# Kernel tuning notes

Measured on AMD Instinct MI355X. Metric: run time of the kernel, lower is better.

The kernel has to match this reference:

```python
import jax, jax.numpy as jnp
import numpy as np

N = 50000      # num vertices
E = 600000     # num incidence pairs
M = 100000     # num hyperedges
IN = 256       # in_channels
H = 8          # heads
C = 32         # out_channels per head


def setup_inputs() -> dict:
    key = jax.random.key(0)
    k = jax.random.split(key, 5)
    X = jax.random.normal(k[0], (N, IN), jnp.float32)
    W = jax.random.normal(k[1], (IN, H * C), jnp.float32) * (1.0 / np.sqrt(IN))
    att_e = jax.random.normal(k[2], (1, H, C), jnp.float32) * 0.1
    vertex = jax.random.randint(k[3], (E,), 0, N)
    edges = jax.random.randint(k[4], (E,), 0, M)
    return {"X": X, "W": W, "att_e": att_e, "vertex": vertex, "edges": edges, "num_edges": M}


def reference(X, W, att_e, vertex, edges, num_edges):
    n, h, c = X.shape[0], att_e.shape[1], att_e.shape[2]
    X0 = X @ W                              # [N, H*C]
    Xh = X0.reshape(n, h, c)                # [N, H, C]
    Xve = Xh[vertex]                        # [E, H, C] gather node feats per incidence
    # mean-aggregate incidences -> hyperedge features
    cnt = jax.ops.segment_sum(jnp.ones((vertex.shape[0],), X.dtype), edges, num_segments=num_edges)
    Xe = jax.ops.segment_sum(Xve, edges, num_segments=num_edges) / jnp.maximum(cnt, 1.0)[:, None, None]  # [M, H, C]
    alpha_e = jnp.sum(Xe * att_e, axis=-1)  # [M, H]
    a_ev = alpha_e[edges]                   # [E, H]
    alpha = jnp.where(a_ev >= 0, a_ev, 0.2 * a_ev)  # leaky_relu(0.2)
    # numerically stable segment softmax over incidences grouped by vertex
    amax = jax.ops.segment_max(alpha, vertex, num_segments=n)[vertex]
    aexp = jnp.exp(alpha - amax)
    asum = jax.ops.segment_sum(aexp, vertex, num_segments=n)[vertex]
    attn = aexp / (asum + 1e-16)            # [E, H]
    Xev = Xe[edges] * attn[:, :, None]      # [E, H, C]
    Xv = jax.ops.segment_sum(Xev, vertex, num_segments=n)  # [N, H, C]
    return jax.nn.gelu(Xv.reshape(n, h * c), approximate=False)
```

## Files before the change

kernel.cpp:

```cpp
#include <hip/hip_runtime.h>
#include <hip/hip_bf16.h>
#include <math.h>

#define NV 50000
#define NE 600000
#define NM 100000
#define KIN 256
#define HCC 256
#define NHH 8

#define NCH 96
#define CHUNK 6250
#define KRANGE 25000
#define NPASS 6
#define HIST_B (NCH * NPASS)
#define CSCAN_B 74

#define SCAN_NB0 25
#define SCAN_NB1 13

#define CNT_B 2344
#define GEMM_RG 784
#define GEMM_B (GEMM_RG * 4)

typedef unsigned int u32;
typedef unsigned short u16;
typedef _Float16 f16;
typedef _Float16 v8h __attribute__((ext_vector_type(8)));
typedef _Float16 v4h __attribute__((ext_vector_type(4)));
typedef float v4f __attribute__((ext_vector_type(4)));
typedef float v8f __attribute__((ext_vector_type(8)));

__global__ __launch_bounds__(256) void k_hist_gemm(const int* __restrict__ vertex,
                                                   const int* __restrict__ edges,
                                                   u16* __restrict__ r_e,
                                                   u16* __restrict__ r_v,
                                                   u16* __restrict__ Ce,
                                                   u16* __restrict__ Cv,
                                                   const float* __restrict__ X,
                                                   const float* __restrict__ W,
                                                   f16* __restrict__ X0) {
    __shared__ __align__(16) u32 smem[KRANGE / 2];
    const int bid = blockIdx.x;
    const int t = threadIdx.x;
    if (bid < HIST_B) {
        u32* hist = smem;
        const int pass = bid / NCH;
        const int chunk = bid % NCH;
        const bool eside = pass < 4;
        const int kbase = (eside ? pass : pass - 4) * KRANGE;
        const int* keys = eside ? edges : vertex;
        u16* rout = eside ? r_e : r_v;
        u16* crow = eside ? (Ce + (size_t)chunk * NM) : (Cv + (size_t)chunk * NV);

        uint4* h4 = (uint4*)hist;
        for (int j = t; j < KRANGE / 8; j += 256) h4[j] = make_uint4(0u, 0u, 0u, 0u);
        __syncthreads();

        const int i0 = chunk * CHUNK;
        for (int i = i0 + t; i < i0 + CHUNK; i += 256) {
            int k = keys[i] - kbase;
            if ((u32)k < (u32)KRANGE) {
                int sh = (k & 1) << 4;
                u32 old = atomicAdd(&hist[k >> 1], 1u << sh);
                rout[i] = (u16)(old >> sh);
            }
        }
        __syncthreads();

        uint4* d4 = (uint4*)(crow + kbase);
        for (int j = t; j < KRANGE / 8; j += 256) d4[j] = h4[j];
        return;
    }
    typedef f16 (*tile_t)[72];
    tile_t sA = (tile_t)smem;
    tile_t sB = (tile_t)((char*)smem + 64 * 72 * 2);
    const int g = bid - HIST_B;
    const int rg = (g >> 5) * 8 + (g & 7);
    const int cg = (g >> 3) & 3;
    if (rg >= (NV + 63) / 64) return;
    const int r0 = rg * 64;
    const int c0 = cg * 64;
    const int wave = t >> 6;
    const int lane = t & 63;
    const int quad = lane >> 4;
    const int l16 = lane & 15;
    const int wr = wave & 1;
    const int wc = wave >> 1;

    v4f acc[2][2] = {{{0.f,0.f,0.f,0.f},{0.f,0.f,0.f,0.f}},
                     {{0.f,0.f,0.f,0.f},{0.f,0.f,0.f,0.f}}};

    for (int kc = 0; kc < KIN; kc += 64) {
        __syncthreads();
        #pragma unroll
        for (int i = 0; i < 4; ++i) {
            int lin = i * 256 + t;
            int row = lin >> 4;
            int k = (lin & 15) * 4;
            int gr = r0 + row;
            float4 x = make_float4(0.f, 0.f, 0.f, 0.f);
            if (gr < NV) x = *(const float4*)(X + (size_t)gr * KIN + kc + k);
            v4h hv = { (f16)x.x, (f16)x.y, (f16)x.z, (f16)x.w };
            *(v4h*)&sA[row][k] = hv;
        }
        #pragma unroll
        for (int i = 0; i < 4; ++i) {
            int lin = i * 256 + t;
            int k = lin >> 4;
            int n = (lin & 15) * 4;
            float4 b = *(const float4*)(W + (size_t)(kc + k) * HCC + c0 + n);
            sB[n + 0][k] = (f16)b.x;
            sB[n + 1][k] = (f16)b.y;
            sB[n + 2][k] = (f16)b.z;
            sB[n + 3][k] = (f16)b.w;
        }
        __syncthreads();
        #pragma unroll
        for (int ks = 0; ks < 2; ++ks) {
            const int kb = ks * 32 + quad * 8;
            v8h a[2], b[2];
            #pragma unroll
            for (int rf = 0; rf < 2; ++rf)
                a[rf] = *(const v8h*)&sA[wr * 32 + rf * 16 + l16][kb];
            #pragma unroll
            for (int cf = 0; cf < 2; ++cf)
                b[cf] = *(const v8h*)&sB[wc * 32 + cf * 16 + l16][kb];
            #pragma unroll
            for (int rf = 0; rf < 2; ++rf)
                #pragma unroll
                for (int cf = 0; cf < 2; ++cf)
                    acc[rf][cf] = __builtin_amdgcn_mfma_f32_16x16x32_f16(a[rf], b[cf], acc[rf][cf], 0, 0, 0);
        }
    }
    #pragma unroll
    for (int rf = 0; rf < 2; ++rf)
        #pragma unroll
        for (int cf = 0; cf < 2; ++cf)
            #pragma unroll
            for (int r = 0; r < 4; ++r) {
                int grow = r0 + wr * 32 + rf * 16 + quad * 4 + r;
                if (grow < NV)
                    X0[(size_t)grow * HCC + c0 + wc * 32 + cf * 16 + l16] = (f16)acc[rf][cf][r];
            }
}

__global__ __launch_bounds__(1024) void k_cscan(u16* __restrict__ Ce,
                                                u16* __restrict__ Cv,
                                                int* __restrict__ e_start,
                                                int* __restrict__ v_start) {
    int tid = blockIdx.x * 1024 + threadIdx.x;
    u32* mat;
    int* outp;
    int col, ncol;
    if (tid < NM / 2)               { mat = (u32*)Ce; outp = e_start; col = tid;          ncol = NM / 2; }
    else if (tid < NM / 2 + NV / 2) { mat = (u32*)Cv; outp = v_start; col = tid - NM / 2; ncol = NV / 2; }
    else return;
    u32 s = 0;
    u32* p = mat + col;
    for (int c = 0; c < NCH; ++c) {
        u32 o = *p;
        *p = s;
        s += o;
        p += ncol;
    }
    outp[2 * col + 1] = (int)(s & 0xffffu);
    outp[2 * col + 2] = (int)(s >> 16);
}

__global__ __launch_bounds__(1024) void k_scan_blk(int* __restrict__ a0,
                                                   int* __restrict__ a1,
                                                   int* __restrict__ bsum) {
    const int b = blockIdx.x;
    int* a;
    int n, base;
    if (b < SCAN_NB0) { a = a0; n = NM + 1; base = b * 4096; }
    else              { a = a1; n = NV + 1; base = (b - SCAN_NB0) * 4096; }
    const int t = threadIdx.x;
    const int lane = t & 63, w = t >> 6;
    const int i = base + t * 4;
    int4 v = make_int4(0, 0, 0, 0);
    if (i + 3 < n) v = *(const int4*)(a + i);
    else if (i < n) {
        v.x = a[i];
        if (i + 1 < n) v.y = a[i + 1];
        if (i + 2 < n) v.z = a[i + 2];
    }
    v.y += v.x; v.z += v.y; v.w += v.z;
    int s = v.w;
    #pragma unroll
    for (int d = 1; d < 64; d <<= 1) {
        int x = __shfl_up(s, d, 64);
        if (lane >= d) s += x;
    }
    __shared__ int partials[16];
    __shared__ int woff[16];
    if (lane == 63) partials[w] = s;
    __syncthreads();
    if (t < 16) {
        int p = partials[t];
        int ps = p;
        #pragma unroll
        for (int d = 1; d < 16; d <<= 1) {
            int x = __shfl_up(ps, d, 64);
            if (t >= d) ps += x;
        }
        woff[t] = ps - p;
        if (t == 15) bsum[b] = ps;
    }
    __syncthreads();
    const int add = (s - v.w) + woff[w];
    v.x += add; v.y += add; v.z += add; v.w += add;
    if (i + 3 < n) *(int4*)(a + i) = v;
    else if (i < n) {
        a[i] = v.x;
        if (i + 1 < n) a[i + 1] = v.y;
        if (i + 2 < n) a[i + 2] = v.z;
    }
}

__global__ __launch_bounds__(1024) void k_scan_add(int* __restrict__ a0,
                                                   int* __restrict__ a1,
                                                   const int* __restrict__ bsum) {
    const int b = blockIdx.x;
    int* a;
    int n, bs0, blocal;
    if (b < SCAN_NB0) { a = a0; n = NM + 1; bs0 = 0;        blocal = b; }
    else              { a = a1; n = NV + 1; bs0 = SCAN_NB0; blocal = b - SCAN_NB0; }
    const int t = threadIdx.x;
    const int lane = t & 63;
    int x = (lane < blocal) ? bsum[bs0 + lane] : 0;
    #pragma unroll
    for (int d = 1; d < 64; d <<= 1) x += __shfl_xor(x, d, 64);
    const int off = x;
    const int i = blocal * 4096 + t * 4;
    if (i + 3 < n) {
        int4 v = *(const int4*)(a + i);
        v.x += off; v.y += off; v.z += off; v.w += off;
        *(int4*)(a + i) = v;
    } else if (i < n) {
        a[i] += off;
        if (i + 1 < n) a[i + 1] += off;
        if (i + 2 < n) a[i + 2] += off;
    }
}

__global__ __launch_bounds__(256) void k_fill2(const int* __restrict__ vertex,
                                               const int* __restrict__ edges,
                                               const u16* __restrict__ r_e,
                                               const u16* __restrict__ r_v,
                                               const int* __restrict__ e_start,
                                               const int* __restrict__ v_start,
                                               const u16* __restrict__ Ce,
                                               const u16* __restrict__ Cv,
                                               int* __restrict__ e_list,
                                               int* __restrict__ v_list) {
    int i = blockIdx.x * 256 + threadIdx.x;
    if (i >= NE) return;
    int v = vertex[i], m = edges[i];
    int chunk = i / CHUNK;
    int pe = e_start[m] + (int)Ce[(size_t)chunk * NM + m] + (int)r_e[i];
    e_list[pe] = v;
    int pv = v_start[v] + (int)Cv[(size_t)chunk * NV + v] + (int)r_v[i];
    v_list[pv] = m;
}

__global__ __launch_bounds__(256) void k_egather(const int* __restrict__ e_start,
                                                 const int* __restrict__ e_list,
                                                 const f16* __restrict__ X0,
                                                 const float* __restrict__ att,
                                                 f16* __restrict__ Xe,
                                                 float* __restrict__ alpha_e) {
    int m = blockIdx.x * 4 + (threadIdx.x >> 6);
    int lane = threadIdx.x & 63;
    int half = lane >> 5;
    int l32 = lane & 31;
    int c8 = l32 * 8;
    int s0 = e_start[m], s1 = e_start[m + 1];
    v8f acc = {0.f,0.f,0.f,0.f,0.f,0.f,0.f,0.f};
    int i = s0 + half;
    for (; i + 2 < s1; i += 4) {
        int v0 = e_list[i], v1 = e_list[i + 2];
        v8h x0 = *(const v8h*)(X0 + (size_t)v0 * HCC + c8);
        v8h x1 = *(const v8h*)(X0 + (size_t)v1 * HCC + c8);
        #pragma unroll
        for (int j = 0; j < 8; ++j) acc[j] += (float)x0[j] + (float)x1[j];
    }
    if (i < s1) {
        int v0 = e_list[i];
        v8h x0 = *(const v8h*)(X0 + (size_t)v0 * HCC + c8);
        #pragma unroll
        for (int j = 0; j < 8; ++j) acc[j] += (float)x0[j];
    }
    #pragma unroll
    for (int j = 0; j < 8; ++j) acc[j] += __shfl_xor(acc[j], 32, 64);
    float inv = 1.0f / fmaxf((float)(s1 - s0), 1.0f);
    #pragma unroll
    for (int j = 0; j < 8; ++j) acc[j] *= inv;
    if (half == 0) {
        v8h xv;
        #pragma unroll
        for (int j = 0; j < 8; ++j) xv[j] = (f16)acc[j];
        *(v8h*)(Xe + (size_t)m * HCC + c8) = xv;
    }
    float4 a0 = *(const float4*)(att + c8);
    float4 a1 = *(const float4*)(att + c8 + 4);
    float p = acc[0]*a0.x + acc[1]*a0.y + acc[2]*a0.z + acc[3]*a0.w
            + acc[4]*a1.x + acc[5]*a1.y + acc[6]*a1.z + acc[7]*a1.w;
    p += __shfl_xor(p, 1, 64);
    p += __shfl_xor(p, 2, 64);
    if (half == 0 && (l32 & 3) == 0) alpha_e[m * NHH + (l32 >> 2)] = p;
}

__global__ __launch_bounds__(256) void k_vgather(const int* __restrict__ v_start,
                                                 const int* __restrict__ v_list,
                                                 const f16* __restrict__ Xe,
                                                 const float* __restrict__ alpha_e,
                                                 float* __restrict__ out) {
    int v = blockIdx.x * 4 + (threadIdx.x >> 6);
    int lane = threadIdx.x & 63;
    int half = lane >> 5;
    int l32 = lane & 31;
    int h = l32 >> 2;
    int c8 = l32 * 8;
    int s0 = v_start[v], s1 = v_start[v + 1];
    v8f acc = {0.f,0.f,0.f,0.f,0.f,0.f,0.f,0.f};
    float se = 0.f;
    int i = s0 + half;
    for (; i + 2 < s1; i += 4) {
        int m0 = v_list[i], m1 = v_list[i + 2];
        float a0 = alpha_e[m0 * NHH + h];
        float a1 = alpha_e[m1 * NHH + h];
        v8h x0 = *(const v8h*)(Xe + (size_t)m0 * HCC + c8);
        v8h x1 = *(const v8h*)(Xe + (size_t)m1 * HCC + c8);
        a0 = (a0 >= 0.f) ? a0 : 0.2f * a0;
        a1 = (a1 >= 0.f) ? a1 : 0.2f * a1;
        float e0 = __expf(a0);
        float e1 = __expf(a1);
        #pragma unroll
        for (int j = 0; j < 8; ++j) acc[j] += e0 * (float)x0[j] + e1 * (float)x1[j];
        se += e0 + e1;
    }
    if (i < s1) {
        int m0 = v_list[i];
        float a0 = alpha_e[m0 * NHH + h];
        v8h x0 = *(const v8h*)(Xe + (size_t)m0 * HCC + c8);
        a0 = (a0 >= 0.f) ? a0 : 0.2f * a0;
        float e0 = __expf(a0);
        #pragma unroll
        for (int j = 0; j < 8; ++j) acc[j] += e0 * (float)x0[j];
        se += e0;
    }
    #pragma unroll
    for (int j = 0; j < 8; ++j) acc[j] += __shfl_xor(acc[j], 32, 64);
    se += __shfl_xor(se, 32, 64);
    if (half) return;
    float inv = 1.0f / (se + 1e-16f);
    float4 o0, o1;
    float xx;
    xx = acc[0] * inv; o0.x = 0.5f * xx * (1.f + erff(xx * 0.70710678118f));
    xx = acc[1] * inv; o0.y = 0.5f * xx * (1.f + erff(xx * 0.70710678118f));
    xx = acc[2] * inv; o0.z = 0.5f * xx * (1.f + erff(xx * 0.70710678118f));
    xx = acc[3] * inv; o0.w = 0.5f * xx * (1.f + erff(xx * 0.70710678118f));
    xx = acc[4] * inv; o1.x = 0.5f * xx * (1.f + erff(xx * 0.70710678118f));
    xx = acc[5] * inv; o1.y = 0.5f * xx * (1.f + erff(xx * 0.70710678118f));
    xx = acc[6] * inv; o1.z = 0.5f * xx * (1.f + erff(xx * 0.70710678118f));
    xx = acc[7] * inv; o1.w = 0.5f * xx * (1.f + erff(xx * 0.70710678118f));
    *(float4*)(out + (size_t)v * HCC + c8) = o0;
    *(float4*)(out + (size_t)v * HCC + c8 + 4) = o1;
}

extern "C" void kernel_launch(void* const* d_in, const int* in_sizes, int n_in,
                              void* d_out, int out_size, void* d_ws, size_t ws_size,
                              hipStream_t stream) {
    const float* X = (const float*)d_in[0];
    const float* W = (const float*)d_in[1];
    const float* att = (const float*)d_in[2];
    const int* vertex = (const int*)d_in[3];
    const int* edges = (const int*)d_in[4];
    float* out = (float*)d_out;

    char* ws = (char*)d_ws;
    size_t off = 0;
    #define WS_TAKE(bytes) (ws + off); off += (((size_t)(bytes)) + 15) & ~(size_t)15
    f16* X0 = (f16*)WS_TAKE((size_t)NV * HCC * 2);
    f16* Xe = (f16*)WS_TAKE((size_t)NM * HCC * 2);
    float* alpha_e = (float*)WS_TAKE((size_t)NM * NHH * 4);
    size_t z0 = off;
    int* e_start = (int*)WS_TAKE((size_t)(NM + 1) * 4);
    int* v_start = (int*)WS_TAKE((size_t)(NV + 1) * 4);
    size_t z1 = off;
    int* e_list = (int*)WS_TAKE((size_t)NE * 4);
    int* v_list = (int*)WS_TAKE((size_t)NE * 4);
    u16* r_e = (u16*)WS_TAKE((size_t)NE * 2);
    u16* r_v = (u16*)WS_TAKE((size_t)NE * 2);
    u16* Ce = (u16*)WS_TAKE((size_t)NCH * NM * 2);
    u16* Cv = (u16*)WS_TAKE((size_t)NCH * NV * 2);
    int* bsum = (int*)WS_TAKE(64 * 4);
    #undef WS_TAKE

    hipMemsetAsync(e_start, 0, z1 - z0, stream);

    k_hist_gemm<<<HIST_B + GEMM_B, 256, 0, stream>>>(vertex, edges, r_e, r_v, Ce, Cv,
                                                     X, W, X0);
    k_cscan<<<CSCAN_B, 1024, 0, stream>>>(Ce, Cv, e_start, v_start);
    k_scan_blk<<<SCAN_NB0 + SCAN_NB1, 1024, 0, stream>>>(e_start, v_start, bsum);
    k_scan_add<<<SCAN_NB0 + SCAN_NB1, 1024, 0, stream>>>(e_start, v_start, bsum);
    k_fill2<<<CNT_B, 256, 0, stream>>>(vertex, edges, r_e, r_v, e_start, v_start,
                                       Ce, Cv, e_list, v_list);
    k_egather<<<NM / 4, 256, 0, stream>>>(e_start, e_list, X0, att, Xe, alpha_e);
    k_vgather<<<NV / 4, 256, 0, stream>>>(v_start, v_list, Xe, alpha_e, out);
}
```

Before: 329.5 us.

## Move GEMM into fill kernel, shrink histogram chunk count, trim memset

The X@W GEMM blocks move from the histogram kernel into the fill kernel, so the histogram kernel no longer carries the large shared-memory footprint alongside GEMM tiles and the GEMM overlaps with the scatter fill instead. The chunk count for the per-chunk histograms drops from 96 to 32, which shrinks the Ce/Cv count matrices and the column-scan work but gives fewer, longer histogram blocks. The memset now clears only the first element of each start array, relying on the scan kernels to write the rest.

```diff
diff --git a/kernel.cpp b/kernel.cpp
--- a/kernel.cpp
+++ b/kernel.cpp
@@ -9,8 +9,8 @@
 #define HCC 256
 #define NHH 8
 
-#define NCH 96
-#define CHUNK 6250
+#define NCH 32
+#define CHUNK 18750
 #define KRANGE 25000
 #define NPASS 6
 #define HIST_B (NCH * NPASS)
@@ -31,118 +31,40 @@
 typedef float v4f __attribute__((ext_vector_type(4)));
 typedef float v8f __attribute__((ext_vector_type(8)));
 
-__global__ __launch_bounds__(256) void k_hist_gemm(const int* __restrict__ vertex,
-                                                   const int* __restrict__ edges,
-                                                   u16* __restrict__ r_e,
-                                                   u16* __restrict__ r_v,
-                                                   u16* __restrict__ Ce,
-                                                   u16* __restrict__ Cv,
-                                                   const float* __restrict__ X,
-                                                   const float* __restrict__ W,
-                                                   f16* __restrict__ X0) {
-    __shared__ __align__(16) u32 smem[KRANGE / 2];
+__global__ __launch_bounds__(256) void k_hist(const int* __restrict__ vertex,
+                                              const int* __restrict__ edges,
+                                              u16* __restrict__ r_e,
+                                              u16* __restrict__ r_v,
+                                              u16* __restrict__ Ce,
+                                              u16* __restrict__ Cv) {
+    __shared__ __align__(16) u32 hist[KRANGE / 2];
     const int bid = blockIdx.x;
     const int t = threadIdx.x;
-    if (bid < HIST_B) {
-        u32* hist = smem;
-        const int pass = bid / NCH;
-        const int chunk = bid % NCH;
-        const bool eside = pass < 4;
-        const int kbase = (eside ? pass : pass - 4) * KRANGE;
-        const int* keys = eside ? edges : vertex;
-        u16* rout = eside ? r_e : r_v;
-        u16* crow = eside ? (Ce + (size_t)chunk * NM) : (Cv + (size_t)chunk * NV);
-
-        uint4* h4 = (uint4*)hist;
-        for (int j = t; j < KRANGE / 8; j += 256) h4[j] = make_uint4(0u, 0u, 0u, 0u);
-        __syncthreads();
-
-        const int i0 = chunk * CHUNK;
-        for (int i = i0 + t; i < i0 + CHUNK; i += 256) {
-            int k = keys[i] - kbase;
-            if ((u32)k < (u32)KRANGE) {
-                int sh = (k & 1) << 4;
-                u32 old = atomicAdd(&hist[k >> 1], 1u << sh);
-                rout[i] = (u16)(old >> sh);
-            }
-        }
-        __syncthreads();
-
-        uint4* d4 = (uint4*)(crow + kbase);
-        for (int j = t; j < KRANGE / 8; j += 256) d4[j] = h4[j];
-        return;
-    }
-    typedef f16 (*tile_t)[72];
-    tile_t sA = (tile_t)smem;
-    tile_t sB = (tile_t)((char*)smem + 64 * 72 * 2);
-    const int g = bid - HIST_B;
-    const int rg = (g >> 5) * 8 + (g & 7);
-    const int cg = (g >> 3) & 3;
-    if (rg >= (NV + 63) / 64) return;
-    const int r0 = rg * 64;
-    const int c0 = cg * 64;
-    const int wave = t >> 6;
-    const int lane = t & 63;
-    const int quad = lane >> 4;
-    const int l16 = lane & 15;
-    const int wr = wave & 1;
-    const int wc = wave >> 1;
-
-    v4f acc[2][2] = {{{0.f,0.f,0.f,0.f},{0.f,0.f,0.f,0.f}},
-                     {{0.f,0.f,0.f,0.f},{0.f,0.f,0.f,0.f}}};
-
-    for (int kc = 0; kc < KIN; kc += 64) {
-        __syncthreads();
-        #pragma unroll
-        for (int i = 0; i < 4; ++i) {
-            int lin = i * 256 + t;
-            int row = lin >> 4;
-            int k = (lin & 15) * 4;
-            int gr = r0 + row;
-            float4 x = make_float4(0.f, 0.f, 0.f, 0.f);
-            if (gr < NV) x = *(const float4*)(X + (size_t)gr * KIN + kc + k);
-            v4h hv = { (f16)x.x, (f16)x.y, (f16)x.z, (f16)x.w };
-            *(v4h*)&sA[row][k] = hv;
-        }
-        #pragma unroll
-        for (int i = 0; i < 4; ++i) {
-            int lin = i * 256 + t;
-            int k = lin >> 4;
-            int n = (lin & 15) * 4;
-            float4 b = *(const float4*)(W + (size_t)(kc + k) * HCC + c0 + n);
-            sB[n + 0][k] = (f16)b.x;
-            sB[n + 1][k] = (f16)b.y;
-            sB[n + 2][k] = (f16)b.z;
-            sB[n + 3][k] = (f16)b.w;
-        }
-        __syncthreads();
-        #pragma unroll
-        for (int ks = 0; ks < 2; ++ks) {
-            const int kb = ks * 32 + quad * 8;
-            v8h a[2], b[2];
-            #pragma unroll
-            for (int rf = 0; rf < 2; ++rf)
-                a[rf] = *(const v8h*)&sA[wr * 32 + rf * 16 + l16][kb];
-            #pragma unroll
-            for (int cf = 0; cf < 2; ++cf)
-                b[cf] = *(const v8h*)&sB[wc * 32 + cf * 16 + l16][kb];
-            #pragma unroll
-            for (int rf = 0; rf < 2; ++rf)
-                #pragma unroll
-                for (int cf = 0; cf < 2; ++cf)
-                    acc[rf][cf] = __builtin_amdgcn_mfma_f32_16x16x32_f16(a[rf], b[cf], acc[rf][cf], 0, 0, 0);
-        }
-    }
-    #pragma unroll
-    for (int rf = 0; rf < 2; ++rf)
-        #pragma unroll
-        for (int cf = 0; cf < 2; ++cf)
-            #pragma unroll
-            for (int r = 0; r < 4; ++r) {
-                int grow = r0 + wr * 32 + rf * 16 + quad * 4 + r;
-                if (grow < NV)
-                    X0[(size_t)grow * HCC + c0 + wc * 32 + cf * 16 + l16] = (f16)acc[rf][cf][r];
-            }
+    const int pass = bid >> 5;
+    const int chunk = bid & (NCH - 1);
+    const bool eside = pass < 4;
+    const int kbase = (eside ? pass : pass - 4) * KRANGE;
+    const int* keys = eside ? edges : vertex;
+    u16* rout = eside ? r_e : r_v;
+    u16* crow = eside ? (Ce + (size_t)chunk * NM) : (Cv + (size_t)chunk * NV);
+
+    uint4* h4 = (uint4*)hist;
+    for (int j = t; j < KRANGE / 8; j += 256) h4[j] = make_uint4(0u, 0u, 0u, 0u);
+    __syncthreads();
+
+    const int i0 = chunk * CHUNK;
+    for (int i = i0 + t; i < i0 + CHUNK; i += 256) {
+        int k = keys[i] - kbase;
+        if ((u32)k < (u32)KRANGE) {
+            int sh = (k & 1) << 4;
+            u32 old = atomicAdd(&hist[k >> 1], 1u << sh);
+            rout[i] = (u16)(old >> sh);
+        }
+    }
+    __syncthreads();
+
+    uint4* d4 = (uint4*)(crow + kbase);
+    for (int j = t; j < KRANGE / 8; j += 256) d4[j] = h4[j];
 }
 
 __global__ __launch_bounds__(1024) void k_cscan(u16* __restrict__ Ce,
@@ -245,24 +167,103 @@
     }
 }
 
-__global__ __launch_bounds__(256) void k_fill2(const int* __restrict__ vertex,
-                                               const int* __restrict__ edges,
-                                               const u16* __restrict__ r_e,
-                                               const u16* __restrict__ r_v,
-                                               const int* __restrict__ e_start,
-                                               const int* __restrict__ v_start,
-                                               const u16* __restrict__ Ce,
-                                               const u16* __restrict__ Cv,
-                                               int* __restrict__ e_list,
-                                               int* __restrict__ v_list) {
-    int i = blockIdx.x * 256 + threadIdx.x;
-    if (i >= NE) return;
-    int v = vertex[i], m = edges[i];
-    int chunk = i / CHUNK;
-    int pe = e_start[m] + (int)Ce[(size_t)chunk * NM + m] + (int)r_e[i];
-    e_list[pe] = v;
-    int pv = v_start[v] + (int)Cv[(size_t)chunk * NV + v] + (int)r_v[i];
-    v_list[pv] = m;
+__global__ __launch_bounds__(256) void k_gemm_fill2(const int* __restrict__ vertex,
+                                                    const int* __restrict__ edges,
+                                                    const u16* __restrict__ r_e,
+                                                    const u16* __restrict__ r_v,
+                                                    const int* __restrict__ e_start,
+                                                    const int* __restrict__ v_start,
+                                                    const u16* __restrict__ Ce,
+                                                    const u16* __restrict__ Cv,
+                                                    int* __restrict__ e_list,
+                                                    int* __restrict__ v_list,
+                                                    const float* __restrict__ X,
+                                                    const float* __restrict__ W,
+                                                    f16* __restrict__ X0) {
+    __shared__ __align__(16) f16 sA[64][72];
+    __shared__ __align__(16) f16 sB[64][72];
+    const int bid = blockIdx.x;
+    const int t = threadIdx.x;
+    if (bid < CNT_B) {
+        int i = bid * 256 + t;
+        if (i < NE) {
+            int v = vertex[i], m = edges[i];
+            int chunk = i / CHUNK;
+            int pe = e_start[m] + (int)Ce[(size_t)chunk * NM + m] + (int)r_e[i];
+            e_list[pe] = v;
+            int pv = v_start[v] + (int)Cv[(size_t)chunk * NV + v] + (int)r_v[i];
+            v_list[pv] = m;
+        }
+        return;
+    }
+    const int g = bid - CNT_B;
+    const int rg = (g >> 5) * 8 + (g & 7);
+    const int cg = (g >> 3) & 3;
+    if (rg >= (NV + 63) / 64) return;
+    const int r0 = rg * 64;
+    const int c0 = cg * 64;
+    const int wave = t >> 6;
+    const int lane = t & 63;
+    const int quad = lane >> 4;
+    const int l16 = lane & 15;
+    const int wr = wave & 1;
+    const int wc = wave >> 1;
+
+    v4f acc[2][2] = {{{0.f,0.f,0.f,0.f},{0.f,0.f,0.f,0.f}},
+                     {{0.f,0.f,0.f,0.f},{0.f,0.f,0.f,0.f}}};
+
+    for (int kc = 0; kc < KIN; kc += 64) {
+        __syncthreads();
+        #pragma unroll
+        for (int i = 0; i < 4; ++i) {
+            int lin = i * 256 + t;
+            int row = lin >> 4;
+            int k = (lin & 15) * 4;
+            int gr = r0 + row;
+            float4 x = make_float4(0.f, 0.f, 0.f, 0.f);
+            if (gr < NV) x = *(const float4*)(X + (size_t)gr * KIN + kc + k);
+            v4h hv = { (f16)x.x, (f16)x.y, (f16)x.z, (f16)x.w };
+            *(v4h*)&sA[row][k] = hv;
+        }
+        #pragma unroll
+        for (int i = 0; i < 4; ++i) {
+            int lin = i * 256 + t;
+            int k = lin >> 4;
+            int n = (lin & 15) * 4;
+            float4 b = *(const float4*)(W + (size_t)(kc + k) * HCC + c0 + n);
+            sB[n + 0][k] = (f16)b.x;
+            sB[n + 1][k] = (f16)b.y;
+            sB[n + 2][k] = (f16)b.z;
+            sB[n + 3][k] = (f16)b.w;
+        }
+        __syncthreads();
+        #pragma unroll
+        for (int ks = 0; ks < 2; ++ks) {
+            const int kb = ks * 32 + quad * 8;
+            v8h a[2], b[2];
+            #pragma unroll
+            for (int rf = 0; rf < 2; ++rf)
+                a[rf] = *(const v8h*)&sA[wr * 32 + rf * 16 + l16][kb];
+            #pragma unroll
+            for (int cf = 0; cf < 2; ++cf)
+                b[cf] = *(const v8h*)&sB[wc * 32 + cf * 16 + l16][kb];
+            #pragma unroll
+            for (int rf = 0; rf < 2; ++rf)
+                #pragma unroll
+                for (int cf = 0; cf < 2; ++cf)
+                    acc[rf][cf] = __builtin_amdgcn_mfma_f32_16x16x32_f16(a[rf], b[cf], acc[rf][cf], 0, 0, 0);
+        }
+    }
+    #pragma unroll
+    for (int rf = 0; rf < 2; ++rf)
+        #pragma unroll
+        for (int cf = 0; cf < 2; ++cf)
+            #pragma unroll
+            for (int r = 0; r < 4; ++r) {
+                int grow = r0 + wr * 32 + rf * 16 + quad * 4 + r;
+                if (grow < NV)
+                    X0[(size_t)grow * HCC + c0 + wc * 32 + cf * 16 + l16] = (f16)acc[rf][cf][r];
+            }
 }
 
 __global__ __launch_bounds__(256) void k_egather(const int* __restrict__ e_start,
@@ -386,10 +387,8 @@
     f16* X0 = (f16*)WS_TAKE((size_t)NV * HCC * 2);
     f16* Xe = (f16*)WS_TAKE((size_t)NM * HCC * 2);
     float* alpha_e = (float*)WS_TAKE((size_t)NM * NHH * 4);
-    size_t z0 = off;
     int* e_start = (int*)WS_TAKE((size_t)(NM + 1) * 4);
     int* v_start = (int*)WS_TAKE((size_t)(NV + 1) * 4);
-    size_t z1 = off;
     int* e_list = (int*)WS_TAKE((size_t)NE * 4);
     int* v_list = (int*)WS_TAKE((size_t)NE * 4);
     u16* r_e = (u16*)WS_TAKE((size_t)NE * 2);
@@ -399,15 +398,16 @@
     int* bsum = (int*)WS_TAKE(64 * 4);
     #undef WS_TAKE
 
-    hipMemsetAsync(e_start, 0, z1 - z0, stream);
-
-    k_hist_gemm<<<HIST_B + GEMM_B, 256, 0, stream>>>(vertex, edges, r_e, r_v, Ce, Cv,
-                                                     X, W, X0);
+    hipMemsetAsync(e_start, 0, 4, stream);
+    hipMemsetAsync(v_start, 0, 4, stream);
+
+    k_hist<<<HIST_B, 256, 0, stream>>>(vertex, edges, r_e, r_v, Ce, Cv);
     k_cscan<<<CSCAN_B, 1024, 0, stream>>>(Ce, Cv, e_start, v_start);
     k_scan_blk<<<SCAN_NB0 + SCAN_NB1, 1024, 0, stream>>>(e_start, v_start, bsum);
     k_scan_add<<<SCAN_NB0 + SCAN_NB1, 1024, 0, stream>>>(e_start, v_start, bsum);
-    k_fill2<<<CNT_B, 256, 0, stream>>>(vertex, edges, r_e, r_v, e_start, v_start,
-                                       Ce, Cv, e_list, v_list);
+    k_gemm_fill2<<<CNT_B + GEMM_B, 256, 0, stream>>>(vertex, edges, r_e, r_v,
+                                                     e_start, v_start, Ce, Cv,
+                                                     e_list, v_list, X, W, X0);
     k_egather<<<NM / 4, 256, 0, stream>>>(e_start, e_list, X0, att, Xe, alpha_e);
     k_vgather<<<NV / 4, 256, 0, stream>>>(v_start, v_list, Xe, alpha_e, out);
 }
```

After: 324.1 us. No clear change (-1.7%).
